# Optimization experiments

Hardware: AMD Instinct MI355X
Metric: run time of the kernel (lower is better)

The kernel has to match this reference:

```python
import jax, jax.numpy as jnp
import numpy as np

USER_NUM = 100000
ITEM_NUM = 150000
N_NODES = USER_NUM + ITEM_NUM
EMB = 64
N_LAYERS = 3
N_EDGES = 1200000


def setup_inputs() -> dict:
    key = jax.random.key(0)
    k1, k2, k3, k4, k5 = jax.random.split(key, 5)
    user_emb = jax.random.normal(k1, (USER_NUM, EMB), dtype=jnp.float32) * 0.1
    item_emb = jax.random.normal(k2, (ITEM_NUM, EMB), dtype=jnp.float32) * 0.1
    adj_rows = jax.random.randint(k3, (N_EDGES,), 0, N_NODES, dtype=jnp.int32)
    adj_cols = jax.random.randint(k4, (N_EDGES,), 0, N_NODES, dtype=jnp.int32)
    # normalized-adjacency-like positive values
    adj_vals = jax.random.uniform(k5, (N_EDGES,), dtype=jnp.float32) * 0.1
    return {"user_emb": user_emb, "item_emb": item_emb,
            "adj_rows": adj_rows, "adj_cols": adj_cols, "adj_vals": adj_vals}


def _spmm(rows, cols, vals, embeds):
    # out[r] += vals[e] * embeds[cols[e]]  — torch.spmm(adj, embeds) with COO adj
    msgs = vals[:, None] * embeds[cols]           # [E, d]
    return jax.ops.segment_sum(msgs, rows, num_segments=N_NODES)


def reference(user_emb, item_emb, adj_rows, adj_cols, adj_vals):
    # forward_graphcl: concat embeddings, n_layers spmm hops, sum all hop outputs
    embeds = jnp.concatenate([user_emb, item_emb], axis=0)  # [N, d]
    main = embeds
    cur = embeds
    for _ in range(N_LAYERS):
        cur = _spmm(adj_rows, adj_cols, adj_vals, cur)
        main = main + cur
    return main
```

## Files before the change

### kernel.cpp

```cpp
#include <hip/hip_runtime.h>
#include <hip/hip_fp16.h>

#define USER_NUM 100000
#define ITEM_NUM 150000
#define N_NODES  250000
#define EMB      64
#define N_EDGES  1200000
#define N_ELEM   (N_NODES * EMB)

#define NBLK1 512
#define NBUCK 245
#define CAP   8192
#define TB1   4096
#define INIT_BLOCKS 3907

__global__ __launch_bounds__(256) void bin_kernel(
    const int* __restrict__ rows, const int* __restrict__ cols,
    const float* __restrict__ vals,
    int* __restrict__ chunkcur, int* __restrict__ bucket_cnt,
    int2* __restrict__ tmp)
{
    __shared__ int  scnt[256];
    __shared__ int  spref[256];
    __shared__ int  schunk[NBUCK];
    __shared__ int2 tilebuf[TB1];

    int b = blockIdx.x, t = threadIdx.x;
    int e0 = (int)((long long)b * N_EDGES / NBLK1);
    int e1 = (int)((long long)(b + 1) * N_EDGES / NBLK1);

    scnt[t] = 0;
    __syncthreads();
    for (int e = e0 + t; e < e1; e += 256)
        atomicAdd(&scnt[rows[e] >> 10], 1);
    __syncthreads();
    int realc = (t < NBUCK) ? scnt[t] : 0;
    int v     = (realc + 7) & ~7;
    __syncthreads();
    spref[t] = v;
    __syncthreads();
    for (int off = 1; off < 256; off <<= 1) {
        int u = (t >= off) ? spref[t - off] : 0;
        __syncthreads();
        spref[t] += u;
        __syncthreads();
    }
    int excl = spref[t] - v;
    __syncthreads();
    spref[t] = excl;
    __syncthreads();
    int padded_total = spref[NBUCK];
    if (t < NBUCK) {
        schunk[t] = (v > 0) ? atomicAdd(&chunkcur[t], v >> 3) : 0;
        if (realc > 0) atomicAdd(&bucket_cnt[t], realc);
    }
    __syncthreads();
    scnt[t] = spref[t];
    for (int j = t; j < padded_total; j += 256)
        tilebuf[j] = make_int2(-1, 0);
    __syncthreads();
    for (int e = e0 + t; e < e1; e += 256) {
        int r  = rows[e];
        int lp = atomicAdd(&scnt[r >> 10], 1);
        tilebuf[lp] = make_int2(((r & 1023) << 18) | cols[e], __float_as_int(vals[e]));
    }
    __syncthreads();
    for (int j = t; j < padded_total; j += 256) {
        int lo = 0, hi = NBUCK;
        while (hi - lo > 1) {
            int mid = (lo + hi) >> 1;
            if (spref[mid] <= j) lo = mid; else hi = mid;
        }
        tmp[(size_t)lo * CAP + schunk[lo] * 8 + (j - spref[lo])] = tilebuf[j];
    }
}

__global__ void scan245_kernel(const int* __restrict__ bucket_cnt,
                               int* __restrict__ bucket_base,
                               int* __restrict__ row_ptr)
{
    __shared__ int s[256];
    int t = threadIdx.x;
    int v = (t < NBUCK) ? bucket_cnt[t] : 0;
    s[t] = v;
    __syncthreads();
    for (int off = 1; off < 256; off <<= 1) {
        int u = (t >= off) ? s[t - off] : 0;
        __syncthreads();
        s[t] += u;
        __syncthreads();
    }
    if (t <= NBUCK) bucket_base[t] = s[t] - v;
    if (t == 0) row_ptr[N_NODES] = N_EDGES;
}

__global__ __launch_bounds__(256) void place_init_kernel(
    const int* __restrict__ chunkcur, const int* __restrict__ bucket_base,
    const int2* __restrict__ tmp,
    int* __restrict__ row_ptr, int2* __restrict__ edges,
    const float* __restrict__ user, const float* __restrict__ item,
    __half* __restrict__ emb16)
{
    __shared__ int  shist[1024];
    __shared__ int  swave[256];
    __shared__ int2 sstage[CAP];

    int t = threadIdx.x;
    if (blockIdx.x >= NBUCK) {
        int gi = (blockIdx.x - NBUCK) * 256 + t;
        if (gi < N_ELEM / 16) {
            int base = gi * 16;
            const int UE = USER_NUM * EMB;
            const float4* src = (base < UE) ? (const float4*)(user + base)
                                            : (const float4*)(item + (base - UE));
            float4 f0 = src[0], f1 = src[1], f2 = src[2], f3 = src[3];
            union { int4 v; __half2 h[4]; } a, b;
            a.h[0] = __float22half2_rn(make_float2(f0.x, f0.y));
            a.h[1] = __float22half2_rn(make_float2(f0.z, f0.w));
            a.h[2] = __float22half2_rn(make_float2(f1.x, f1.y));
            a.h[3] = __float22half2_rn(make_float2(f1.z, f1.w));
            b.h[0] = __float22half2_rn(make_float2(f2.x, f2.y));
            b.h[1] = __float22half2_rn(make_float2(f2.z, f2.w));
            b.h[2] = __float22half2_rn(make_float2(f3.x, f3.y));
            b.h[3] = __float22half2_rn(make_float2(f3.z, f3.w));
            ((int4*)(emb16 + base))[0] = a.v;
            ((int4*)(emb16 + base))[1] = b.v;
        }
        return;
    }

    int b = blockIdx.x;
    int nrec = chunkcur[b] * 8;
    const int2* src = tmp + (size_t)b * CAP;

    for (int i = t; i < 1024; i += 256) shist[i] = 0;
    __syncthreads();
    for (int j = t; j < nrec; j += 256) {
        int x = src[j].x;
        if (x != -1) atomicAdd(&shist[x >> 18], 1);
    }
    __syncthreads();
    int h0 = shist[4 * t], h1 = shist[4 * t + 1], h2 = shist[4 * t + 2], h3 = shist[4 * t + 3];
    int sum = h0 + h1 + h2 + h3;
    swave[t] = sum;
    __syncthreads();
    for (int off = 1; off < 256; off <<= 1) {
        int u = (t >= off) ? swave[t - off] : 0;
        __syncthreads();
        swave[t] += u;
        __syncthreads();
    }
    int base = swave[t] - sum;
    __syncthreads();
    shist[4 * t]     = base;
    shist[4 * t + 1] = base + h0;
    shist[4 * t + 2] = base + h0 + h1;
    shist[4 * t + 3] = base + h0 + h1 + h2;
    __syncthreads();
    int bb = bucket_base[b];
    for (int i = t; i < 1024; i += 256) {
        int idx = b * 1024 + i;
        if (idx < N_NODES) row_ptr[idx] = bb + shist[i];
    }
    __syncthreads();
    for (int j = t; j < nrec; j += 256) {
        int2 rec = src[j];
        if (rec.x != -1) {
            int lp = atomicAdd(&shist[rec.x >> 18], 1);
            sstage[lp] = make_int2(rec.x & 0x3FFFF, rec.y);
        }
    }
    __syncthreads();
    int cnt = bucket_base[b + 1] - bb;
    for (int j = t; j < cnt; j += 256)
        edges[bb + j] = sstage[j];
}

template <int MODE>
__global__ __launch_bounds__(256) void spmm_kernel(
    const int* __restrict__ row_ptr, const int2* __restrict__ edges,
    const __half* __restrict__ in16, const __half* __restrict__ emb16,
    const __half* __restrict__ cur1,
    float* __restrict__ out, __half* __restrict__ cur_out)
{
    int t = blockIdx.x * blockDim.x + threadIdx.x;
    int r = t >> 4;
    int l = t & 15;
    if (r >= N_NODES) return;
    int start = row_ptr[r];
    int end   = row_ptr[r + 1];
    int idx   = r * EMB + 4 * l;

    union { int2 i; __half2 h[2]; } pe, p1, p2;
    if (MODE == 1) {
        pe.i = *(const int2*)(emb16 + idx);
        p1.i = *(const int2*)(cur1 + idx);
        p2.i = *(const int2*)(in16 + idx);
    }

    float ax = 0.f, ay = 0.f, az = 0.f, aw = 0.f;
    for (int j = start; j < end; j += 8) {
        int2 e[8];
#pragma unroll
        for (int k = 0; k < 8; ++k) e[k] = edges[j + k];
#pragma unroll
        for (int k = 0; k < 8; ++k) {
            bool ok = (j + k < end);
            int   c = ok ? e[k].x : 0;
            float v = ok ? __int_as_float(e[k].y) : 0.0f;
            union { int2 i; __half2 h[2]; } g;
            g.i = *(const int2*)(in16 + c * EMB + 4 * l);
            float2 x0 = __half22float2(g.h[0]);
            float2 x1 = __half22float2(g.h[1]);
            ax += v * x0.x; ay += v * x0.y;
            az += v * x1.x; aw += v * x1.y;
        }
    }

    if (MODE == 0) {
        union { int2 i; __half2 h[2]; } o;
        o.h[0] = __float22half2_rn(make_float2(ax, ay));
        o.h[1] = __float22half2_rn(make_float2(az, aw));
        *(int2*)(cur_out + idx) = o.i;
    } else {
        float2 e0 = __half22float2(pe.h[0]), e1 = __half22float2(pe.h[1]);
        float2 c0 = __half22float2(p1.h[0]), c1 = __half22float2(p1.h[1]);
        float2 d0 = __half22float2(p2.h[0]), d1 = __half22float2(p2.h[1]);
        float4 o = make_float4(e0.x + c0.x + d0.x + ax,
                               e0.y + c0.y + d0.y + ay,
                               e1.x + c1.x + d1.x + az,
                               e1.y + c1.y + d1.y + aw);
        *(float4*)(out + idx) = o;
    }
}

extern "C" void kernel_launch(void* const* d_in, const int* in_sizes, int n_in,
                              void* d_out, int out_size, void* d_ws, size_t ws_size,
                              hipStream_t stream) {
    const float* user = (const float*)d_in[0];
    const float* item = (const float*)d_in[1];
    const int*   rows = (const int*)d_in[2];
    const int*   cols = (const int*)d_in[3];
    const float* vals = (const float*)d_in[4];
    float*       out  = (float*)d_out;

    char* p = (char*)d_ws;
    __half* emb16    = (__half*)p;  p += (size_t)N_ELEM * 2;
    __half* cur1     = (__half*)p;  p += (size_t)N_ELEM * 2;
    __half* cur2     = (__half*)p;  p += (size_t)N_ELEM * 2;
    int2*   tmp      = (int2*)p;    p += (size_t)NBUCK * CAP * 8;
    int2*   edges    = (int2*)p;    p += (size_t)N_EDGES * 8 + 256;
    int*    row_ptr  = (int*)p;     p += 1000448;
    int*    bucket_base = (int*)p;  p += 1024;
    int*    bucket_cnt  = (int*)p;  p += 1024;
    int*    chunkcur    = (int*)p;  p += 1024;

    hipMemsetAsync(bucket_cnt, 0, 2048, stream);

    bin_kernel<<<NBLK1, 256, 0, stream>>>(rows, cols, vals, chunkcur, bucket_cnt, tmp);
    scan245_kernel<<<1, 256, 0, stream>>>(bucket_cnt, bucket_base, row_ptr);
    place_init_kernel<<<NBUCK + INIT_BLOCKS, 256, 0, stream>>>(
        chunkcur, bucket_base, tmp, row_ptr, edges, user, item, emb16);

    const int spmm_blocks = (N_NODES * 16 + 255) / 256;
    spmm_kernel<0><<<spmm_blocks, 256, 0, stream>>>(row_ptr, edges, emb16, emb16, cur1, out, cur1);
    spmm_kernel<0><<<spmm_blocks, 256, 0, stream>>>(row_ptr, edges, cur1, emb16, cur1, out, cur2);
    spmm_kernel<1><<<spmm_blocks, 256, 0, stream>>>(row_ptr, edges, cur2, emb16, cur1, out, nullptr);
}
```

Before: 282.8 us.

## Fuse embedding conversion into binning kernel and fold bucket scan into place kernel

Moves the fp32-to-fp16 embedding conversion blocks from the place kernel into the binning kernel, and drops the separate single-block scan kernel by having each place block redo the 245-entry prefix scan itself. This removes one kernel launch and lets the conversion overlap with binning. The per-tile binary search for a bucket is replaced by a shared byte array mapping each slot to its bucket, padding fill is done per bucket, and the conversion loads now use nontemporal loads. The cost is a redundant scan in every place block and heavier shared memory use in the binning kernel.

Result: no change. 279.8 us (-1.1%).

```diff
diff --git a/kernel.cpp b/kernel.cpp
--- a/kernel.cpp
+++ b/kernel.cpp
@@ -14,107 +14,37 @@
 #define TB1   4096
 #define INIT_BLOCKS 3907
 
-__global__ __launch_bounds__(256) void bin_kernel(
+typedef float f4 __attribute__((ext_vector_type(4)));
+typedef int   i4 __attribute__((ext_vector_type(4)));
+
+__global__ __launch_bounds__(256) void bin_init_kernel(
     const int* __restrict__ rows, const int* __restrict__ cols,
     const float* __restrict__ vals,
     int* __restrict__ chunkcur, int* __restrict__ bucket_cnt,
-    int2* __restrict__ tmp)
+    int2* __restrict__ tmp,
+    const float* __restrict__ user, const float* __restrict__ item,
+    __half* __restrict__ emb16)
 {
     __shared__ int  scnt[256];
     __shared__ int  spref[256];
     __shared__ int  schunk[NBUCK];
+    __shared__ unsigned char sbuck[TB1];
     __shared__ int2 tilebuf[TB1];
 
-    int b = blockIdx.x, t = threadIdx.x;
-    int e0 = (int)((long long)b * N_EDGES / NBLK1);
-    int e1 = (int)((long long)(b + 1) * N_EDGES / NBLK1);
-
-    scnt[t] = 0;
-    __syncthreads();
-    for (int e = e0 + t; e < e1; e += 256)
-        atomicAdd(&scnt[rows[e] >> 10], 1);
-    __syncthreads();
-    int realc = (t < NBUCK) ? scnt[t] : 0;
-    int v     = (realc + 7) & ~7;
-    __syncthreads();
-    spref[t] = v;
-    __syncthreads();
-    for (int off = 1; off < 256; off <<= 1) {
-        int u = (t >= off) ? spref[t - off] : 0;
-        __syncthreads();
-        spref[t] += u;
-        __syncthreads();
-    }
-    int excl = spref[t] - v;
-    __syncthreads();
-    spref[t] = excl;
-    __syncthreads();
-    int padded_total = spref[NBUCK];
-    if (t < NBUCK) {
-        schunk[t] = (v > 0) ? atomicAdd(&chunkcur[t], v >> 3) : 0;
-        if (realc > 0) atomicAdd(&bucket_cnt[t], realc);
-    }
-    __syncthreads();
-    scnt[t] = spref[t];
-    for (int j = t; j < padded_total; j += 256)
-        tilebuf[j] = make_int2(-1, 0);
-    __syncthreads();
-    for (int e = e0 + t; e < e1; e += 256) {
-        int r  = rows[e];
-        int lp = atomicAdd(&scnt[r >> 10], 1);
-        tilebuf[lp] = make_int2(((r & 1023) << 18) | cols[e], __float_as_int(vals[e]));
-    }
-    __syncthreads();
-    for (int j = t; j < padded_total; j += 256) {
-        int lo = 0, hi = NBUCK;
-        while (hi - lo > 1) {
-            int mid = (lo + hi) >> 1;
-            if (spref[mid] <= j) lo = mid; else hi = mid;
-        }
-        tmp[(size_t)lo * CAP + schunk[lo] * 8 + (j - spref[lo])] = tilebuf[j];
-    }
-}
-
-__global__ void scan245_kernel(const int* __restrict__ bucket_cnt,
-                               int* __restrict__ bucket_base,
-                               int* __restrict__ row_ptr)
-{
-    __shared__ int s[256];
     int t = threadIdx.x;
-    int v = (t < NBUCK) ? bucket_cnt[t] : 0;
-    s[t] = v;
-    __syncthreads();
-    for (int off = 1; off < 256; off <<= 1) {
-        int u = (t >= off) ? s[t - off] : 0;
-        __syncthreads();
-        s[t] += u;
-        __syncthreads();
-    }
-    if (t <= NBUCK) bucket_base[t] = s[t] - v;
-    if (t == 0) row_ptr[N_NODES] = N_EDGES;
-}
-
-__global__ __launch_bounds__(256) void place_init_kernel(
-    const int* __restrict__ chunkcur, const int* __restrict__ bucket_base,
-    const int2* __restrict__ tmp,
-    int* __restrict__ row_ptr, int2* __restrict__ edges,
-    const float* __restrict__ user, const float* __restrict__ item,
-    __half* __restrict__ emb16)
-{
-    __shared__ int  shist[1024];
-    __shared__ int  swave[256];
-    __shared__ int2 sstage[CAP];
-
-    int t = threadIdx.x;
-    if (blockIdx.x >= NBUCK) {
-        int gi = (blockIdx.x - NBUCK) * 256 + t;
+
+    if (blockIdx.x >= NBLK1) {
+        int gi = (blockIdx.x - NBLK1) * 256 + t;
         if (gi < N_ELEM / 16) {
             int base = gi * 16;
             const int UE = USER_NUM * EMB;
-            const float4* src = (base < UE) ? (const float4*)(user + base)
-                                            : (const float4*)(item + (base - UE));
-            float4 f0 = src[0], f1 = src[1], f2 = src[2], f3 = src[3];
-            union { int4 v; __half2 h[4]; } a, b;
+            const f4* src = (base < UE) ? (const f4*)(user + base)
+                                        : (const f4*)(item + (base - UE));
+            f4 f0 = __builtin_nontemporal_load(src);
+            f4 f1 = __builtin_nontemporal_load(src + 1);
+            f4 f2 = __builtin_nontemporal_load(src + 2);
+            f4 f3 = __builtin_nontemporal_load(src + 3);
+            union { i4 v; __half2 h[4]; } a, b;
             a.h[0] = __float22half2_rn(make_float2(f0.x, f0.y));
             a.h[1] = __float22half2_rn(make_float2(f0.z, f0.w));
             a.h[2] = __float22half2_rn(make_float2(f1.x, f1.y));
@@ -123,13 +53,89 @@
             b.h[1] = __float22half2_rn(make_float2(f2.z, f2.w));
             b.h[2] = __float22half2_rn(make_float2(f3.x, f3.y));
             b.h[3] = __float22half2_rn(make_float2(f3.z, f3.w));
-            ((int4*)(emb16 + base))[0] = a.v;
-            ((int4*)(emb16 + base))[1] = b.v;
+            ((i4*)(emb16 + base))[0] = a.v;
+            ((i4*)(emb16 + base))[1] = b.v;
         }
         return;
     }
 
     int b = blockIdx.x;
+    int e0 = (int)((long long)b * N_EDGES / NBLK1);
+    int e1 = (int)((long long)(b + 1) * N_EDGES / NBLK1);
+
+    scnt[t] = 0;
+    __syncthreads();
+    for (int e = e0 + t; e < e1; e += 256)
+        atomicAdd(&scnt[rows[e] >> 10], 1);
+    __syncthreads();
+    int realc = (t < NBUCK) ? scnt[t] : 0;
+    int v     = (realc + 7) & ~7;
+    __syncthreads();
+    spref[t] = v;
+    __syncthreads();
+    for (int off = 1; off < 256; off <<= 1) {
+        int u = (t >= off) ? spref[t - off] : 0;
+        __syncthreads();
+        spref[t] += u;
+        __syncthreads();
+    }
+    int excl = spref[t] - v;
+    __syncthreads();
+    spref[t] = excl;
+    __syncthreads();
+    int padded_total = spref[NBUCK];
+
+    scnt[t] = excl;
+    if (t < NBUCK) {
+        schunk[t] = (v > 0) ? atomicAdd(&chunkcur[t], v >> 3) : 0;
+        if (realc > 0) atomicAdd(&bucket_cnt[t], realc);
+        for (int k = realc; k < v; ++k) tilebuf[excl + k] = make_int2(-1, 0);
+        for (int k = 0; k < v; ++k) sbuck[excl + k] = (unsigned char)t;
+    }
+    __syncthreads();
+    for (int e = e0 + t; e < e1; e += 256) {
+        int r  = rows[e];
+        int lp = atomicAdd(&scnt[r >> 10], 1);
+        tilebuf[lp] = make_int2(((r & 1023) << 18) | cols[e], __float_as_int(vals[e]));
+    }
+    __syncthreads();
+    for (int j = t; j < padded_total; j += 256) {
+        int lo = sbuck[j];
+        tmp[(size_t)lo * CAP + schunk[lo] * 8 + (j - spref[lo])] = tilebuf[j];
+    }
+}
+
+__global__ __launch_bounds__(256) void place_kernel(
+    const int* __restrict__ chunkcur, const int* __restrict__ bucket_cnt,
+    const int2* __restrict__ tmp,
+    int* __restrict__ row_ptr, int2* __restrict__ edges)
+{
+    __shared__ int  shist[1024];
+    __shared__ int  swave[256];
+    __shared__ int  sbase[2];
+    __shared__ int2 sstage[CAP];
+
+    int t = threadIdx.x;
+    int b = blockIdx.x;
+
+    int vv = (t < NBUCK) ? bucket_cnt[t] : 0;
+    swave[t] = vv;
+    __syncthreads();
+    for (int off = 1; off < 256; off <<= 1) {
+        int u = (t >= off) ? swave[t - off] : 0;
+        __syncthreads();
+        swave[t] += u;
+        __syncthreads();
+    }
+    if (t == 0) {
+        sbase[0] = (b == 0) ? 0 : swave[b - 1];
+        sbase[1] = swave[b];
+        if (b == 0) row_ptr[N_NODES] = N_EDGES;
+    }
+    __syncthreads();
+    int bb  = sbase[0];
+    int cnt = sbase[1] - sbase[0];
+
     int nrec = chunkcur[b] * 8;
     const int2* src = tmp + (size_t)b * CAP;
 
@@ -157,7 +163,6 @@
     shist[4 * t + 2] = base + h0 + h1;
     shist[4 * t + 3] = base + h0 + h1 + h2;
     __syncthreads();
-    int bb = bucket_base[b];
     for (int i = t; i < 1024; i += 256) {
         int idx = b * 1024 + i;
         if (idx < N_NODES) row_ptr[idx] = bb + shist[i];
@@ -171,7 +176,6 @@
         }
     }
     __syncthreads();
-    int cnt = bucket_base[b + 1] - bb;
     for (int j = t; j < cnt; j += 256)
         edges[bb + j] = sstage[j];
 }
@@ -257,10 +261,9 @@
 
     hipMemsetAsync(bucket_cnt, 0, 2048, stream);
 
-    bin_kernel<<<NBLK1, 256, 0, stream>>>(rows, cols, vals, chunkcur, bucket_cnt, tmp);
-    scan245_kernel<<<1, 256, 0, stream>>>(bucket_cnt, bucket_base, row_ptr);
-    place_init_kernel<<<NBUCK + INIT_BLOCKS, 256, 0, stream>>>(
-        chunkcur, bucket_base, tmp, row_ptr, edges, user, item, emb16);
+    bin_init_kernel<<<NBLK1 + INIT_BLOCKS, 256, 0, stream>>>(
+        rows, cols, vals, chunkcur, bucket_cnt, tmp, user, item, emb16);
+    place_kernel<<<NBUCK, 256, 0, stream>>>(chunkcur, bucket_cnt, tmp, row_ptr, edges);
 
     const int spmm_blocks = (N_NODES * 16 + 255) / 256;
     spmm_kernel<0><<<spmm_blocks, 256, 0, stream>>>(row_ptr, edges, emb16, emb16, cur1, out, cur1);
```
